# Optimization experiments

Hardware: AMD Instinct MI355X
Metric: run time of the kernel (lower is better)

Reference implementation:

```python
import jax, jax.numpy as jnp
import numpy as np

HID = 2048
NH = 16
HD = HID // NH  # 128
EPS = 1e-6
BASE = 10000.0


def _rmsnorm(x, w):
    xf = x.astype(jnp.float32)
    y = xf * jax.lax.rsqrt(jnp.mean(xf * xf, axis=-1, keepdims=True) + EPS)
    return y.astype(x.dtype) * w


def _rope_cos_sin(seq_len, dtype):
    inv_freq = 1.0 / (BASE ** (jnp.arange(0, HD, 2, dtype=jnp.float32) / HD))
    t = jnp.arange(seq_len, dtype=jnp.float32)
    freqs = jnp.outer(t, inv_freq)          # [S, HD/2]
    emb = jnp.concatenate([freqs, freqs], axis=-1)  # [S, HD]
    return jnp.cos(emb).astype(dtype), jnp.sin(emb).astype(dtype)


def _rotate_half(x):
    x1, x2 = jnp.split(x, 2, axis=-1)
    return jnp.concatenate([-x2, x1], axis=-1)


def setup_inputs() -> dict:
    key = jax.random.key(0)
    ks = jax.random.split(key, 8)
    B, S = 2, 2048
    s = 0.02
    return {
        "hidden_states": jax.random.normal(ks[0], (B, S, HID), jnp.float32),
        "Wq": jax.random.normal(ks[1], (HID, HID), jnp.float32) * s,
        "Wk": jax.random.normal(ks[2], (HID, HID), jnp.float32) * s,
        "Wv": jax.random.normal(ks[3], (HID, HID), jnp.float32) * s,
        "Wo": jax.random.normal(ks[4], (HID, HID), jnp.float32) * s,
        "w1": jax.random.normal(ks[5], (HID, HID), jnp.float32) * s,
        "w2": jax.random.normal(ks[6], (HID, HID), jnp.float32) * s,
        "w3": jax.random.normal(ks[7], (HID, HID), jnp.float32) * s,
        "ln1_w": jnp.ones((HID,), jnp.float32),
        "ln2_w": jnp.ones((HID,), jnp.float32),
    }


def reference(hidden_states, Wq, Wk, Wv, Wo, w1, w2, w3, ln1_w, ln2_w):
    B, S, _ = hidden_states.shape
    residual = hidden_states
    x = _rmsnorm(hidden_states, ln1_w)

    # projections -> [B, NH, S, HD]
    q = (x @ Wq).reshape(B, S, NH, HD).transpose(0, 2, 1, 3)
    k = (x @ Wk).reshape(B, S, NH, HD).transpose(0, 2, 1, 3)
    v = (x @ Wv).reshape(B, S, NH, HD).transpose(0, 2, 1, 3)

    cos, sin = _rope_cos_sin(S, x.dtype)  # [S, HD]
    cos = cos[None, None]  # broadcast over batch and heads
    sin = sin[None, None]
    q = q * cos + _rotate_half(q) * sin
    k = k * cos + _rotate_half(k) * sin

    scores = jnp.einsum("bhqd,bhkd->bhqk", q, k) / np.sqrt(HD).astype(np.float32)
    # no attention_mask (torch default path). fp32 softmax.
    attn = jax.nn.softmax(scores.astype(jnp.float32), axis=-1).astype(q.dtype)
    ctx = jnp.einsum("bhqk,bhkd->bhqd", attn, v)  # [B, NH, S, HD]
    ctx = ctx.transpose(0, 2, 1, 3).reshape(B, S, HID)
    attn_out = ctx @ Wo

    h = residual + attn_out
    residual = h
    y = _rmsnorm(h, ln2_w)
    mlp = (jax.nn.silu(y @ w1) * (y @ w3)) @ w2
    return residual + mlp
```

## Files before the change

kernel.cpp:

```cpp
#include <hip/hip_runtime.h>

#define HIDN 2048
#define NHEAD 16
#define HD 128
#define SEQ 2048
#define BATCH 2
#define NROWS (BATCH*SEQ)

typedef __bf16 bf16_t;
typedef bf16_t bf16x8 __attribute__((ext_vector_type(8)));
typedef float f32x4 __attribute__((ext_vector_type(4)));

#define AS1 __attribute__((address_space(1)))
#define AS3 __attribute__((address_space(3)))

__device__ __forceinline__ unsigned short f2bf(float x) {
  union { bf16_t b; unsigned short u; } cv; cv.b = (bf16_t)x; return cv.u;
}

#define MFMA16(a,b,c) __builtin_amdgcn_mfma_f32_16x16x32_bf16((a),(b),(c),0,0,0)

__device__ __forceinline__ void gload16(const void* g, void* l) {
  __builtin_amdgcn_global_load_lds((const AS1 void*)g, (AS3 void*)l, 16, 0, 0);
}

__global__ __launch_bounds__(256) void transpose_all_kernel(
    const float* __restrict__ Wq, const float* __restrict__ Wk,
    const float* __restrict__ Wv, const float* __restrict__ Wo,
    const float* __restrict__ w1, const float* __restrict__ w3,
    const float* __restrict__ w2, unsigned short* __restrict__ wblk) {
  const int z = blockIdx.z;
  const float* W; unsigned short* dstb; int tmode = 0, half = 0;
  switch (z) {
    case 0: W = Wq; dstb = wblk;                       tmode = 1; break;
    case 1: W = Wk; dstb = wblk + (size_t)2048 * HIDN; tmode = 1; break;
    case 2: W = Wv; dstb = wblk + (size_t)4096 * HIDN; break;
    case 3: W = Wo; dstb = wblk + (size_t)6144 * HIDN; break;
    case 4: W = w1; dstb = wblk + (size_t)8192 * HIDN; tmode = 2; half = 0; break;
    case 5: W = w3; dstb = wblk + (size_t)8192 * HIDN; tmode = 2; half = 1; break;
    default: W = w2; dstb = wblk + (size_t)12288 * HIDN; break;
  }
  __shared__ float t[64][69];
  const int tid = threadIdx.x;
  const int bn = blockIdx.x * 64, bk = blockIdx.y * 64;
  const int lc = (tid & 15) * 4, lrw = tid >> 4;
#pragma unroll
  for (int i = 0; i < 4; ++i) {
    int k = bk + lrw + i * 16;
    float4 v = *(const float4*)(W + (long)k * HIDN + bn + lc);
    t[lrw + i * 16][lc] = v.x; t[lrw + i * 16][lc + 1] = v.y;
    t[lrw + i * 16][lc + 2] = v.z; t[lrw + i * 16][lc + 3] = v.w;
  }
  __syncthreads();
  const int nl = tid >> 2, k0 = (tid & 3) * 16;
  int n = bn + nl;
  int dst;
  if (tmode == 0) dst = n;
  else if (tmode == 1) { int d = n & 127; dst = (n & ~127) | ((d & 63) << 1) | (d >> 6); }
  else dst = (n >> 4) * 32 + half * 16 + (n & 15);
  unsigned short* orow = dstb + (long)dst * HIDN + bk + k0;
#pragma unroll
  for (int j = 0; j < 16; j += 4) {
    ushort4 o;
    o.x = f2bf(t[k0 + j][nl]);     o.y = f2bf(t[k0 + j + 1][nl]);
    o.z = f2bf(t[k0 + j + 2][nl]); o.w = f2bf(t[k0 + j + 3][nl]);
    *(ushort4*)(orow + j) = o;
  }
}

__global__ void rope_table_kernel(float* __restrict__ cosT, float* __restrict__ sinT) {
  int s = blockIdx.x, d = threadIdx.x;
  float invf = powf(10000.0f, (-2.0f * (float)d) / 128.0f);
  float ang = (float)s * invf;
  cosT[s * 64 + d] = cosf(ang);
  sinT[s * 64 + d] = sinf(ang);
}

__global__ __launch_bounds__(256) void rmsnorm_kernel(
    const float* __restrict__ x, const float* __restrict__ w, unsigned short* __restrict__ out) {
  long row = blockIdx.x;
  const float* xr = x + row * HIDN;
  int c0 = threadIdx.x * 4;
  float4 v0 = *(const float4*)(xr + c0);
  float4 v1 = *(const float4*)(xr + 1024 + c0);
  float s = v0.x*v0.x + v0.y*v0.y + v0.z*v0.z + v0.w*v0.w
          + v1.x*v1.x + v1.y*v1.y + v1.z*v1.z + v1.w*v1.w;
#pragma unroll
  for (int off = 1; off < 64; off <<= 1) s += __shfl_xor(s, off);
  __shared__ float red[4];
  if ((threadIdx.x & 63) == 0) red[threadIdx.x >> 6] = s;
  __syncthreads();
  float tot = red[0] + red[1] + red[2] + red[3];
  float r = 1.0f / sqrtf(tot * (1.0f / (float)HIDN) + 1e-6f);
  float4 w0 = *(const float4*)(w + c0);
  float4 w1 = *(const float4*)(w + 1024 + c0);
  ushort4 o0, o1;
  o0.x = f2bf(v0.x * r * w0.x); o0.y = f2bf(v0.y * r * w0.y);
  o0.z = f2bf(v0.z * r * w0.z); o0.w = f2bf(v0.w * r * w0.w);
  o1.x = f2bf(v1.x * r * w1.x); o1.y = f2bf(v1.y * r * w1.y);
  o1.z = f2bf(v1.z * r * w1.z); o1.w = f2bf(v1.w * r * w1.w);
  *(ushort4*)(out + row * HIDN + c0) = o0;
  *(ushort4*)(out + row * HIDN + 1024 + c0) = o1;
}

template <int MODE>
__global__ __launch_bounds__(512, 2) void gemm256_kernel(
    const unsigned short* __restrict__ A, const unsigned short* __restrict__ Bt,
    int nbx,
    void* __restrict__ p0, void* __restrict__ p1, void* __restrict__ p2,
    const float* __restrict__ cosT, const float* __restrict__ sinT) {
  __shared__ unsigned short L[65536];
  const int tid = threadIdx.x;
  const int wave = tid >> 6, lane = tid & 63;
  const int lr = lane & 15, lkg = lane >> 4;
  const int wr = wave >> 2, wc = wave & 3;
  const int x7 = lr & 7;
  const int nwg = (int)gridDim.x;
  const int bid = (int)blockIdx.x;
  const int wg = (bid & 7) * (nwg >> 3) + (bid >> 3);
  const int bx = wg % nbx, by = wg / nbx;
  const long bm = (long)by * 256, bn = (long)bx * 256;
  const int sslot = (lane & 7) ^ (lane >> 3);
  const unsigned short* Ag = A + (bm + wave * 8 + (lane >> 3)) * HIDN + sslot * 8;
  const unsigned short* Bg = Bt + (bn + wave * 8 + (lane >> 3)) * HIDN + sslot * 8;
  const char* Lc = (const char*)L;
  f32x4 acc[8][4] = {};
  bf16x8 af[2][2], bfr[4][2];

#define STG(b, mat, half, tile)                                                   \
  {                                                                               \
    const unsigned short* gsrc = ((mat) ? Bg : Ag) + ((long)(half) * 128) * HIDN + (long)(tile) * 64; \
    unsigned short* ldst = &L[((4 * (b) + 2 * (mat) + (half)) * 8192) + wave * 8 * 64]; \
    gload16(gsrc, ldst);                                                          \
    gload16(gsrc + (long)64 * HIDN, ldst + 4096);                                 \
  }
#define DSRA(b, q)                                                                \
  { _Pragma("unroll") for (int mm = 0; mm < 2; ++mm) {                            \
      int row128 = ((q) * 2 + mm) * 16 + lr;                                      \
      _Pragma("unroll") for (int ks = 0; ks < 2; ++ks) {                          \
        int s = ks * 4 + lkg;                                                     \
        af[mm][ks] = *(const bf16x8*)(Lc + (4 * (b) + wr) * 16384 + row128 * 128 + ((s ^ x7) << 4)); \
      } } }
#define DSRB(b)                                                                   \
  { _Pragma("unroll") for (int n = 0; n < 4; ++n) {                               \
      int row128 = (wc & 1) * 64 + n * 16 + lr;                                   \
      _Pragma("unroll") for (int ks = 0; ks < 2; ++ks) {                          \
        int s = ks * 4 + lkg;                                                     \
        bfr[n][ks] = *(const bf16x8*)(Lc + (4 * (b) + 2 + (wc >> 1)) * 16384 + row128 * 128 + ((s ^ x7) << 4)); \
      } } }
#define MFMAQ(q)                                                                  \
  { __builtin_amdgcn_s_setprio(1);                                                \
    _Pragma("unroll") for (int mm = 0; mm < 2; ++mm)                              \
      _Pragma("unroll") for (int n = 0; n < 4; ++n) {                             \
        acc[(q) * 2 + mm][n] = MFMA16(af[mm][0], bfr[n][0], acc[(q) * 2 + mm][n]); \
        acc[(q) * 2 + mm][n] = MFMA16(af[mm][1], bfr[n][1], acc[(q) * 2 + mm][n]); \
      }                                                                           \
    __builtin_amdgcn_s_setprio(0); }
#define BARR __builtin_amdgcn_s_barrier()
#define LGK0 { asm volatile("s_waitcnt lgkmcnt(0)" ::: "memory"); __builtin_amdgcn_sched_barrier(0); }

  STG(0, 0, 0, 0); STG(0, 0, 1, 0); STG(0, 1, 0, 0); STG(0, 1, 1, 0);
  STG(1, 1, 0, 1); STG(1, 1, 1, 1); STG(1, 0, 0, 1);
  asm volatile("s_waitcnt vmcnt(6)" ::: "memory");
  __builtin_amdgcn_sched_barrier(0);
  BARR;

  const int NIT = HIDN / 128;
#pragma unroll 1
  for (int i = 0; i < NIT; ++i) {
    const int t2 = 2 * i + 2, t3 = 2 * i + 3;
    const bool nl_ = (i < NIT - 1);
    DSRA(0, 0); DSRB(0);
    STG(1, 0, 1, 2 * i + 1);
    asm volatile("s_waitcnt lgkmcnt(8)" ::: "memory");
    BARR; LGK0; MFMAQ(0); BARR;
    DSRA(0, 1);
    if (nl_) STG(0, 1, 0, t2);
    BARR; LGK0; MFMAQ(1); BARR;
    DSRA(0, 2);
    if (nl_) STG(0, 1, 1, t2);
    BARR; LGK0; MFMAQ(2); BARR;
    DSRA(0, 3);
    BARR; LGK0; MFMAQ(3);
    if (nl_) { asm volatile("s_waitcnt vmcnt(4)" ::: "memory"); }
    else     { asm volatile("s_waitcnt vmcnt(0)" ::: "memory"); }
    __builtin_amdgcn_sched_barrier(0);
    BARR;
    DSRA(1, 0); DSRB(1);
    if (nl_) STG(0, 0, 0, t2);
    asm volatile("s_waitcnt lgkmcnt(8)" ::: "memory");
    BARR; LGK0; MFMAQ(0); BARR;
    DSRA(1, 1);
    if (nl_) { STG(0, 0, 1, t2); STG(1, 1, 0, t3); }
    BARR; LGK0; MFMAQ(1); BARR;
    DSRA(1, 2);
    if (nl_) STG(1, 1, 1, t3);
    BARR; LGK0; MFMAQ(2); BARR;
    DSRA(1, 3);
    if (nl_) STG(1, 0, 0, t3);
    BARR; LGK0; MFMAQ(3);
    if (nl_) { asm volatile("s_waitcnt vmcnt(6)" ::: "memory"); __builtin_amdgcn_sched_barrier(0); }
    BARR;
  }
#undef STG
#undef DSRA
#undef DSRB
#undef MFMAQ
#undef BARR
#undef LGK0

  const int gc0 = (int)bn + wc * 64;
  if (MODE == 1) {
    unsigned short* bout = (unsigned short*)p0;
#pragma unroll
    for (int m = 0; m < 8; ++m) {
      long r0 = bm + wr * 128 + m * 16 + lkg * 4;
#pragma unroll
      for (int n = 0; n < 4; n += 2) {
        int ggrp = (gc0 + n * 16) >> 5;
        long c = (long)ggrp * 16 + lr;
#pragma unroll
        for (int r = 0; r < 4; ++r) {
          float x = acc[m][n][r], g = acc[m][n + 1][r];
          float sv = x / (1.0f + __expf(-x)) * g;
          bout[(r0 + r) * 2048 + c] = f2bf(sv);
        }
      }
    }
  } else if (MODE == 2 || MODE == 3) {
    float* fout = (float*)p0;
    const float* addsrc = (const float*)p1;
#pragma unroll
    for (int m = 0; m < 8; ++m) {
      long r0 = bm + wr * 128 + m * 16 + lkg * 4;
#pragma unroll
      for (int n = 0; n < 4; ++n) {
        long c = gc0 + n * 16 + lr;
#pragma unroll
        for (int r = 0; r < 4; ++r) {
          long idx = (r0 + r) * 2048 + c;
          if (MODE == 2) fout[idx] = addsrc[idx] + acc[m][n][r];
          else fout[idx] = fout[idx] + acc[m][n][r];
        }
      }
    }
  } else {
    int bufid = gc0 >> 11;
    if (bufid == 2) {
      unsigned short* vT = (unsigned short*)p2;
#pragma unroll
      for (int m = 0; m < 8; ++m) {
        long r0 = bm + wr * 128 + m * 16 + lkg * 4;
        long bq = r0 >> 11;
        int s = (int)(r0 & 2047);
#pragma unroll
        for (int n = 0; n < 4; ++n) {
          int wcol = (gc0 + n * 16 + lr) & 2047;
          int hh = wcol >> 7, dd = wcol & 127;
          ushort4 pw;
          pw.x = f2bf(acc[m][n][0]); pw.y = f2bf(acc[m][n][1]);
          pw.z = f2bf(acc[m][n][2]); pw.w = f2bf(acc[m][n][3]);
          *(ushort4*)(vT + ((bq * 16 + hh) * 128 + dd) * (long)SEQ + s) = pw;
        }
      }
    } else {
      unsigned short* dst = (bufid == 0) ? (unsigned short*)p0 : (unsigned short*)p1;
      const float qscale = (bufid == 0) ? 0.12751689f : 1.0f;
#pragma unroll
      for (int m = 0; m < 8; ++m) {
        long r0 = bm + wr * 128 + m * 16 + lkg * 4;
#pragma unroll
        for (int n = 0; n < 4; ++n) {
          int wcol = (gc0 + n * 16 + lr) & 2047;
          int f = wcol & 127, hh = wcol >> 7;
          int j = f >> 1, odd = f & 1;
          int oc = hh * 128 + (odd ? 64 : 0) + j;
#pragma unroll
          for (int r = 0; r < 4; ++r) {
            long row = r0 + r;
            int s = (int)(row & (SEQ - 1));
            float cv = cosT[s * 64 + j], sn = sinT[s * 64 + j];
            float v = acc[m][n][r];
            float o = __shfl_xor(v, 1);
            float res = (odd ? (v * cv + o * sn) : (v * cv - o * sn)) * qscale;
            dst[row * 2048 + oc] = f2bf(res);
          }
        }
      }
    }
  }
}

__global__ __launch_bounds__(256, 3) void flash_attn_kernel(
    const unsigned short* __restrict__ Q, const unsigned short* __restrict__ Kb,
    const unsigned short* __restrict__ vT, unsigned short* __restrict__ O) {
  __shared__ unsigned short Ks[64 * 128];
  __shared__ unsigned short Vs[128 * 64];
  __shared__ unsigned short Ps[4][16][72];
  const int bid = (int)blockIdx.x;
  const int wg = (bid & 7) * 128 + (bid >> 3);
  const int qt = wg & 31, h = (wg >> 5) & 15, b = wg >> 9;
  const int tid = threadIdx.x, wave = tid >> 6, lane = tid & 63;
  const int lr = lane & 15, lkg = lane >> 4, lk = lkg * 8;
  const long rowbase = (long)b * SEQ;
  const int qrow0 = qt * 64 + wave * 16;
  bf16x8 aq[4];
#pragma unroll
  for (int ks = 0; ks < 4; ++ks)
    aq[ks] = *(const bf16x8*)(Q + (rowbase + qrow0 + lr) * HIDN + h * HD + ks * 32 + lk);
  const unsigned short* vbase = vT + ((long)(b * 16 + h) * 128) * SEQ;
  const int kr_ = tid >> 4, kc_ = tid & 15;
  const int vd_ = tid >> 3, vc_ = tid & 7;
  int4 kreg[4], vreg[4];
  f32x4 acc[8] = {};
  float m_ = -3.0e38f, l_ = 0.f;

#define GLOADKV(kv0_)                                                              \
  { _Pragma("unroll")                                                              \
    for (int j = 0; j < 4; ++j)                                                    \
      kreg[j] = *(const int4*)(Kb + (rowbase + (kv0_) + kr_ + j * 16) * HIDN + h * HD + kc_ * 8); \
    _Pragma("unroll")                                                              \
    for (int j = 0; j < 4; ++j)                                                    \
      vreg[j] = *(const int4*)(vbase + (long)(vd_ + j * 32) * SEQ + (kv0_) + vc_ * 8); }
#define DSWRITEKV()                                                                \
  { _Pragma("unroll")                                                              \
    for (int j = 0; j < 4; ++j) {                                                  \
      int row = kr_ + j * 16;                                                      \
      *(int4*)((char*)Ks + row * 256 + ((kc_ ^ (row & 15)) << 4)) = kreg[j];       \
    }                                                                              \
    _Pragma("unroll")                                                              \
    for (int j = 0; j < 4; ++j) {                                                  \
      int d = vd_ + j * 32;                                                        \
      *(int4*)((char*)Vs + d * 128 + ((vc_ ^ (d & 7)) << 4)) = vreg[j];            \
    } }

  GLOADKV(0);
  asm volatile("s_waitcnt vmcnt(0)" ::: "memory");
  DSWRITEKV();
  asm volatile("s_waitcnt lgkmcnt(0)" ::: "memory");
  __builtin_amdgcn_sched_barrier(0);
  asm volatile("s_barrier" ::: "memory");

  for (int t = 0; t < SEQ / 64; ++t) {
    if (t + 1 < SEQ / 64) GLOADKV((long)(t + 1) * 64);
    const char* ksb = (const char*)Ks;
    f32x4 sa[4] = {};
#pragma unroll
    for (int n = 0; n < 4; ++n) {
      int row = n * 16 + lr;
#pragma unroll
      for (int ks = 0; ks < 4; ++ks) {
        bf16x8 bk = *(const bf16x8*)(ksb + row * 256 + (((ks * 4 + lkg) ^ (row & 15)) << 4));
        sa[n] = MFMA16(bk, aq[ks], sa[n]);
      }
    }
    float pmax = sa[0][0];
#pragma unroll
    for (int n = 0; n < 4; ++n)
#pragma unroll
      for (int r = 0; r < 4; ++r) pmax = fmaxf(pmax, sa[n][r]);
    pmax = fmaxf(pmax, __shfl_xor(pmax, 16));
    pmax = fmaxf(pmax, __shfl_xor(pmax, 32));
    if (__all(pmax - m_ <= 11.54f)) {
      float psum = 0.f;
#pragma unroll
      for (int n = 0; n < 4; ++n)
#pragma unroll
        for (int r = 0; r < 4; ++r) {
          float p = exp2f(sa[n][r] - m_);
          sa[n][r] = p;
          psum += p;
        }
      psum += __shfl_xor(psum, 16);
      psum += __shfl_xor(psum, 32);
      l_ += psum;
    } else {
      float mnew = fmaxf(m_, pmax);
      float corr = exp2f(m_ - mnew);
      float psum = 0.f;
#pragma unroll
      for (int n = 0; n < 4; ++n)
#pragma unroll
        for (int r = 0; r < 4; ++r) {
          float p = exp2f(sa[n][r] - mnew);
          sa[n][r] = p;
          psum += p;
        }
      psum += __shfl_xor(psum, 16);
      psum += __shfl_xor(psum, 32);
      l_ = l_ * corr + psum;
      m_ = mnew;
      float corr4[4];
#pragma unroll
      for (int r = 0; r < 4; ++r) corr4[r] = __shfl(corr, 4 * lkg + r);
#pragma unroll
      for (int df = 0; df < 8; ++df)
#pragma unroll
        for (int r = 0; r < 4; ++r) acc[df][r] *= corr4[r];
    }
#pragma unroll
    for (int n = 0; n < 4; ++n) {
      ushort4 pw;
      pw.x = f2bf(sa[n][0]); pw.y = f2bf(sa[n][1]);
      pw.z = f2bf(sa[n][2]); pw.w = f2bf(sa[n][3]);
      *(ushort4*)&Ps[wave][lr][n * 16 + 4 * lkg] = pw;
    }
    bf16x8 pa0 = *(const bf16x8*)&Ps[wave][lr][lk];
    bf16x8 pa1 = *(const bf16x8*)&Ps[wave][lr][32 + lk];
    const char* vsb = (const char*)Vs;
#pragma unroll
    for (int df = 0; df < 8; ++df) {
      int row = df * 16 + lr;
      int x7 = row & 7;
      bf16x8 bv0 = *(const bf16x8*)(vsb + row * 128 + ((lkg ^ x7) << 4));
      bf16x8 bv1 = *(const bf16x8*)(vsb + row * 128 + (((4 + lkg) ^ x7) << 4));
      acc[df] = MFMA16(pa0, bv0, acc[df]);
      acc[df] = MFMA16(pa1, bv1, acc[df]);
    }
    asm volatile("s_barrier" ::: "memory");
    if (t + 1 < SEQ / 64) {
      asm volatile("s_waitcnt vmcnt(0)" ::: "memory");
      DSWRITEKV();
      asm volatile("s_waitcnt lgkmcnt(0)" ::: "memory");
      __builtin_amdgcn_sched_barrier(0);
      asm volatile("s_barrier" ::: "memory");
    }
  }
#undef GLOADKV
#undef DSWRITEKV
  float invl = 1.0f / l_;
  float invl4[4];
#pragma unroll
  for (int r = 0; r < 4; ++r) invl4[r] = __shfl(invl, 4 * lkg + r);
#pragma unroll
  for (int r = 0; r < 4; ++r) {
    long orow = rowbase + qrow0 + lkg * 4 + r;
#pragma unroll
    for (int df = 0; df < 8; ++df)
      O[orow * HIDN + h * HD + df * 16 + lr] = f2bf(acc[df][r] * invl4[r]);
  }
}

extern "C" void kernel_launch(void* const* d_in, const int* in_sizes, int n_in,
                              void* d_out, int out_size, void* d_ws, size_t ws_size,
                              hipStream_t stream) {
  const float* hidden = (const float*)d_in[0];
  const float* Wq = (const float*)d_in[1];
  const float* Wk = (const float*)d_in[2];
  const float* Wv = (const float*)d_in[3];
  const float* Wo = (const float*)d_in[4];
  const float* w1 = (const float*)d_in[5];
  const float* w2 = (const float*)d_in[6];
  const float* w3 = (const float*)d_in[7];
  const float* ln1 = (const float*)d_in[8];
  const float* ln2 = (const float*)d_in[9];
  float* out = (float*)d_out;

  char* ws = (char*)d_ws;
  size_t off = 0;
  auto alloc = [&](size_t bytes) -> void* {
    void* p = ws + off;
    off += (bytes + 255) & ~(size_t)255;
    return p;
  };
  unsigned short* wblk = (unsigned short*)alloc((size_t)(2048L * 6 + 2048) * HIDN * 2);
  unsigned short* wQ = wblk;
  unsigned short* wG = wblk + (size_t)8192 * HIDN;
  unsigned short* wO = wblk + (size_t)6144 * HIDN;
  unsigned short* wD = wblk + (size_t)12288 * HIDN;
  unsigned short* xb   = (unsigned short*)alloc((size_t)NROWS * HIDN * 2);
  unsigned short* qb   = (unsigned short*)alloc((size_t)NROWS * HIDN * 2);
  unsigned short* kb   = (unsigned short*)alloc((size_t)NROWS * HIDN * 2);
  unsigned short* vTb  = (unsigned short*)alloc((size_t)NROWS * HIDN * 2);
  unsigned short* ctxb = (unsigned short*)alloc((size_t)NROWS * HIDN * 2);
  float* cosT = (float*)alloc((size_t)SEQ * 64 * 4);
  float* sinT = (float*)alloc((size_t)SEQ * 64 * 4);
  if (off > ws_size) return;

  transpose_all_kernel<<<dim3(HIDN / 64, HIDN / 64, 7), 256, 0, stream>>>(
      Wq, Wk, Wv, Wo, w1, w3, w2, wblk);
  rope_table_kernel<<<SEQ, 64, 0, stream>>>(cosT, sinT);

  rmsnorm_kernel<<<NROWS, 256, 0, stream>>>(hidden, ln1, xb);

  gemm256_kernel<0><<<(6144 / 256) * (NROWS / 256), 512, 0, stream>>>(
      xb, wQ, 6144 / 256, qb, kb, vTb, cosT, sinT);

  flash_attn_kernel<<<(SEQ / 64) * NHEAD * BATCH, 256, 0, stream>>>(qb, kb, vTb, ctxb);

  gemm256_kernel<2><<<(2048 / 256) * (NROWS / 256), 512, 0, stream>>>(
      ctxb, wO, 2048 / 256, out, (void*)hidden, nullptr, nullptr, nullptr);

  rmsnorm_kernel<<<NROWS, 256, 0, stream>>>(out, ln2, xb);

  gemm256_kernel<1><<<(4096 / 256) * (NROWS / 256), 512, 0, stream>>>(
      xb, wG, 4096 / 256, qb, nullptr, nullptr, nullptr, nullptr);

  gemm256_kernel<3><<<(2048 / 256) * (NROWS / 256), 512, 0, stream>>>(
      qb, wD, 2048 / 256, out, nullptr, nullptr, nullptr, nullptr);
}
```

Before: 487.8 us.

## Add 128x256-tile GEMM kernel for N=2048 output projections

```diff
diff --git a/kernel.cpp b/kernel.cpp
--- a/kernel.cpp
+++ b/kernel.cpp
@@ -10,6 +10,7 @@
 typedef __bf16 bf16_t;
 typedef bf16_t bf16x8 __attribute__((ext_vector_type(8)));
 typedef float f32x4 __attribute__((ext_vector_type(4)));
+typedef unsigned short ushort8 __attribute__((ext_vector_type(8)));
 
 #define AS1 __attribute__((address_space(1)))
 #define AS3 __attribute__((address_space(3)))
@@ -60,11 +61,11 @@
   else dst = (n >> 4) * 32 + half * 16 + (n & 15);
   unsigned short* orow = dstb + (long)dst * HIDN + bk + k0;
 #pragma unroll
-  for (int j = 0; j < 16; j += 4) {
-    ushort4 o;
-    o.x = f2bf(t[k0 + j][nl]);     o.y = f2bf(t[k0 + j + 1][nl]);
-    o.z = f2bf(t[k0 + j + 2][nl]); o.w = f2bf(t[k0 + j + 3][nl]);
-    *(ushort4*)(orow + j) = o;
+  for (int j = 0; j < 16; j += 8) {
+    ushort8 o;
+#pragma unroll
+    for (int jj = 0; jj < 8; ++jj) o[jj] = f2bf(t[k0 + j + jj][nl]);
+    *(ushort8*)(orow + j) = o;
   }
 }
 
@@ -206,8 +207,6 @@
 #undef DSRA
 #undef DSRB
 #undef MFMAQ
-#undef BARR
-#undef LGK0
 
   const int gc0 = (int)bn + wc * 64;
   if (MODE == 1) {
@@ -224,23 +223,6 @@
           float x = acc[m][n][r], g = acc[m][n + 1][r];
           float sv = x / (1.0f + __expf(-x)) * g;
           bout[(r0 + r) * 2048 + c] = f2bf(sv);
-        }
-      }
-    }
-  } else if (MODE == 2 || MODE == 3) {
-    float* fout = (float*)p0;
-    const float* addsrc = (const float*)p1;
-#pragma unroll
-    for (int m = 0; m < 8; ++m) {
-      long r0 = bm + wr * 128 + m * 16 + lkg * 4;
-#pragma unroll
-      for (int n = 0; n < 4; ++n) {
-        long c = gc0 + n * 16 + lr;
-#pragma unroll
-        for (int r = 0; r < 4; ++r) {
-          long idx = (r0 + r) * 2048 + c;
-          if (MODE == 2) fout[idx] = addsrc[idx] + acc[m][n][r];
-          else fout[idx] = fout[idx] + acc[m][n][r];
         }
       }
     }
@@ -286,6 +268,120 @@
             dst[row * 2048 + oc] = f2bf(res);
           }
         }
+      }
+    }
+  }
+#undef BARR
+#undef LGK0
+}
+
+template <int MODE>
+__global__ __launch_bounds__(512, 2) void gemmWide_kernel(
+    const unsigned short* __restrict__ A, const unsigned short* __restrict__ Bt,
+    void* __restrict__ p0, const void* __restrict__ p1) {
+  __shared__ unsigned short L[49152];
+  const int tid = threadIdx.x;
+  const int wave = tid >> 6, lane = tid & 63;
+  const int lr = lane & 15, lkg = lane >> 4;
+  const int wr = wave >> 2, wc = wave & 3;
+  const int x7 = lr & 7;
+  const int bid = (int)blockIdx.x;
+  const int wg = (bid & 7) * 32 + (bid >> 3);
+  const int bx = wg >> 5, by = wg & 31;
+  const long bm = (long)by * 128, bn = (long)bx * 256;
+  const int sslot = (lane & 7) ^ (lane >> 3);
+  const unsigned short* Ag = A + (bm + wave * 8 + (lane >> 3)) * HIDN + sslot * 8;
+  const unsigned short* Bg = Bt + (bn + wave * 8 + (lane >> 3)) * HIDN + sslot * 8;
+  const char* Lc = (const char*)L;
+  f32x4 acc[4][4] = {};
+  bf16x8 af[2][2], bfr[4][2];
+
+#define STGA(b, tile)                                                             \
+  { const unsigned short* g = Ag + (long)(tile) * 64;                             \
+    unsigned short* d = &L[(b) * 24576 + wave * 8 * 64];                          \
+    gload16(g, d); gload16(g + (long)64 * HIDN, d + 4096); }
+#define STGB(b, hh, tile)                                                         \
+  { const unsigned short* g = Bg + ((long)(hh) * 128) * HIDN + (long)(tile) * 64; \
+    unsigned short* d = &L[(b) * 24576 + 8192 + (hh) * 8192 + wave * 8 * 64];     \
+    gload16(g, d); gload16(g + (long)64 * HIDN, d + 4096); }
+#define DSRA2(b, p)                                                               \
+  { _Pragma("unroll") for (int mm = 0; mm < 2; ++mm) {                            \
+      int row = wr * 64 + ((p) * 2 + mm) * 16 + lr;                               \
+      _Pragma("unroll") for (int ks = 0; ks < 2; ++ks) {                          \
+        int s = ks * 4 + lkg;                                                     \
+        af[mm][ks] = *(const bf16x8*)(Lc + (b) * 49152 + row * 128 + ((s ^ x7) << 4)); \
+      } } }
+#define DSRBW(b)                                                                  \
+  { _Pragma("unroll") for (int n = 0; n < 4; ++n) {                               \
+      int row = wc * 64 + n * 16 + lr;                                            \
+      _Pragma("unroll") for (int ks = 0; ks < 2; ++ks) {                          \
+        int s = ks * 4 + lkg;                                                     \
+        bfr[n][ks] = *(const bf16x8*)(Lc + (b) * 49152 + 16384 + row * 128 + ((s ^ x7) << 4)); \
+      } } }
+#define MFMAP(p)                                                                  \
+  { __builtin_amdgcn_s_setprio(1);                                                \
+    _Pragma("unroll") for (int mm = 0; mm < 2; ++mm)                              \
+      _Pragma("unroll") for (int n = 0; n < 4; ++n) {                             \
+        acc[(p) * 2 + mm][n] = MFMA16(af[mm][0], bfr[n][0], acc[(p) * 2 + mm][n]); \
+        acc[(p) * 2 + mm][n] = MFMA16(af[mm][1], bfr[n][1], acc[(p) * 2 + mm][n]); \
+      }                                                                           \
+    __builtin_amdgcn_s_setprio(0); }
+#define BARR __builtin_amdgcn_s_barrier()
+#define LGK0 { asm volatile("s_waitcnt lgkmcnt(0)" ::: "memory"); __builtin_amdgcn_sched_barrier(0); }
+
+  STGA(0, 0); STGB(0, 0, 0); STGB(0, 1, 0);
+  STGB(1, 0, 1); STGB(1, 1, 1);
+  asm volatile("s_waitcnt vmcnt(4)" ::: "memory");
+  __builtin_amdgcn_sched_barrier(0);
+  BARR;
+
+  const int NIT = HIDN / 128;
+#pragma unroll 1
+  for (int i = 0; i < NIT; ++i) {
+    const int t1 = 2 * i + 1, t2 = 2 * i + 2, t3 = 2 * i + 3;
+    const bool nl_ = (i < NIT - 1);
+    DSRBW(0); DSRA2(0, 0);
+    STGA(1, t1);
+    asm volatile("s_waitcnt lgkmcnt(8)" ::: "memory");
+    BARR; LGK0; MFMAP(0); BARR;
+    DSRA2(0, 1);
+    if (nl_) { STGB(0, 0, t2); STGB(0, 1, t2); }
+    BARR; LGK0; MFMAP(1);
+    if (nl_) { asm volatile("s_waitcnt vmcnt(4)" ::: "memory"); }
+    else     { asm volatile("s_waitcnt vmcnt(0)" ::: "memory"); }
+    __builtin_amdgcn_sched_barrier(0);
+    BARR;
+    DSRBW(1); DSRA2(1, 0);
+    if (nl_) STGA(0, t2);
+    asm volatile("s_waitcnt lgkmcnt(8)" ::: "memory");
+    BARR; LGK0; MFMAP(0); BARR;
+    DSRA2(1, 1);
+    if (nl_) { STGB(1, 0, t3); STGB(1, 1, t3); }
+    BARR; LGK0; MFMAP(1);
+    if (nl_) { asm volatile("s_waitcnt vmcnt(4)" ::: "memory"); __builtin_amdgcn_sched_barrier(0); }
+    BARR;
+  }
+#undef STGA
+#undef STGB
+#undef DSRA2
+#undef DSRBW
+#undef MFMAP
+#undef BARR
+#undef LGK0
+
+  float* fout = (float*)p0;
+  const float* addsrc = (const float*)p1;
+#pragma unroll
+  for (int m = 0; m < 4; ++m) {
+    long r0 = bm + wr * 64 + m * 16 + lkg * 4;
+#pragma unroll
+    for (int n = 0; n < 4; ++n) {
+      long c = bn + wc * 64 + n * 16 + lr;
+#pragma unroll
+      for (int r = 0; r < 4; ++r) {
+        long idx = (r0 + r) * 2048 + c;
+        if (MODE == 2) fout[idx] = addsrc[idx] + acc[m][n][r];
+        else fout[idx] = fout[idx] + acc[m][n][r];
       }
     }
   }
@@ -488,14 +584,12 @@
 
   flash_attn_kernel<<<(SEQ / 64) * NHEAD * BATCH, 256, 0, stream>>>(qb, kb, vTb, ctxb);
 
-  gemm256_kernel<2><<<(2048 / 256) * (NROWS / 256), 512, 0, stream>>>(
-      ctxb, wO, 2048 / 256, out, (void*)hidden, nullptr, nullptr, nullptr);
+  gemmWide_kernel<2><<<256, 512, 0, stream>>>(ctxb, wO, out, hidden);
 
   rmsnorm_kernel<<<NROWS, 256, 0, stream>>>(out, ln2, xb);
 
   gemm256_kernel<1><<<(4096 / 256) * (NROWS / 256), 512, 0, stream>>>(
       xb, wG, 4096 / 256, qb, nullptr, nullptr, nullptr, nullptr);
 
-  gemm256_kernel<3><<<(2048 / 256) * (NROWS / 256), 512, 0, stream>>>(
-      qb, wD, 2048 / 256, out, nullptr, nullptr, nullptr, nullptr);
-}
+  gemmWide_kernel<3><<<256, 512, 0, stream>>>(qb, wD, out, nullptr);
+}
```

New measurement: 445.6 us, median of 2. 1.09x faster.
